# Kernel optimization log

Measured on AMD Instinct MI355X. Metric: run time of the kernel, lower is better.

Reference implementation:

```python
import jax, jax.numpy as jnp
import numpy as np

N, E, D, C = 50000, 800000, 128, 7
BN_EPS = 1e-5


def _sage_conv(x, src, dst, Wl, Wr, b):
    # mean-aggregate neighbor messages per destination, then linear + root linear
    msgs = x[src]  # [E, D] irregular gather
    summed = jax.ops.segment_sum(msgs, dst, num_segments=N)
    cnt = jax.ops.segment_sum(jnp.ones((src.shape[0],), x.dtype), dst, num_segments=N)
    agg = summed / jnp.maximum(cnt, 1.0)[:, None]
    return agg @ Wl.T + x @ Wr.T + b


def _bn_eval(x, g, be):
    # running_mean=0, running_var=1 (eval mode)
    return x * (g / jnp.sqrt(1.0 + BN_EPS)) + be


def setup_inputs() -> dict:
    key = jax.random.key(0)
    ks = jax.random.split(key, 20)
    w = lambda k, s: jax.random.normal(k, s, dtype=jnp.float32) * 0.05
    inp = {
        "x": jax.random.normal(ks[0], (N, D), dtype=jnp.float32),
        "edge_index": jax.random.randint(ks[1], (2, E), 0, N, dtype=jnp.int64),
        "Wl0": w(ks[2], (D, D)), "Wr0": w(ks[3], (D, D)), "b0": jnp.zeros((D,), jnp.float32),
        "Wl1": w(ks[4], (D, D)), "Wr1": w(ks[5], (D, D)), "b1": jnp.zeros((D,), jnp.float32),
        "Wl2": w(ks[6], (D, D)), "Wr2": w(ks[7], (D, D)), "b2": jnp.zeros((D,), jnp.float32),
        "g0": jnp.ones((D,), jnp.float32), "be0": jnp.zeros((D,), jnp.float32),
        "g1": jnp.ones((D,), jnp.float32), "be1": jnp.zeros((D,), jnp.float32),
        "dW1": w(ks[8], (D, D)), "db1": jnp.zeros((D,), jnp.float32),
        "dW2": w(ks[9], (C, D)), "db2": jnp.zeros((C,), jnp.float32),
        "dW3": w(ks[10], (D, D)), "db3": jnp.zeros((D,), jnp.float32),
    }
    return inp


def reference(x, edge_index, Wl0, Wr0, b0, Wl1, Wr1, b1, Wl2, Wr2, b2,
              g0, be0, g1, be1, dW1, db1, dW2, db2, dW3, db3):
    src, dst = edge_index[0], edge_index[1]
    h = _sage_conv(x, src, dst, Wl0, Wr0, b0)
    h = jax.nn.relu(_bn_eval(h, g0, be0))  # dropout is identity in eval
    h = _sage_conv(h, src, dst, Wl1, Wr1, b1)
    h = jax.nn.relu(_bn_eval(h, g1, be1))
    h = _sage_conv(h, src, dst, Wl2, Wr2, b2)
    recon_x1 = h @ dW1.T + db1
    recon_x2 = h @ dW2.T + db2
    recon_x3 = h @ dW3.T + db3
    return (recon_x1, recon_x2, recon_x3)
```

## Files before the change

kernel.cpp:

```cpp
#include <hip/hip_runtime.h>
#include <hip/hip_fp16.h>

static constexpr float kBnEps = 1e-5f;
static constexpr int MAXB = 1024;

typedef __attribute__((ext_vector_type(8))) _Float16 f16x8;
typedef __attribute__((ext_vector_type(4))) float f32x4;

__global__ void detect_k(const int* __restrict__ eb, int* __restrict__ flag) {
    int l = threadIdx.x;
    int v = eb[2 * l + 1];
    unsigned long long m = __ballot(v == 0);
    if (l == 0) flag[0] = (m == ~0ull) ? 1 : 0;
}

__device__ __forceinline__ int edge_src(const int* eb, int is64, int E, int e) {
    return is64 ? eb[2 * e] : eb[e];
}
__device__ __forceinline__ int edge_dst(const int* eb, int is64, int E, int e) {
    return is64 ? eb[2 * E + 2 * e] : eb[E + e];
}

__global__ __launch_bounds__(256) void histA_k(const int* __restrict__ eb,
                                               const int* __restrict__ flag,
                                               int* __restrict__ gcnt, int E,
                                               int nbuck) {
    __shared__ int lh[MAXB];
    for (int i = threadIdx.x; i < nbuck; i += 256) lh[i] = 0;
    __syncthreads();
    int is64 = flag[0];
    int base = blockIdx.x * 4096;
#pragma unroll
    for (int i = 0; i < 16; ++i) {
        int e = base + i * 256 + threadIdx.x;
        if (e < E) {
            int d = edge_dst(eb, is64, E, e);
            atomicAdd(&lh[d >> 7], 1);
        }
    }
    __syncthreads();
    for (int i = threadIdx.x; i < nbuck; i += 256) {
        int c = lh[i];
        if (c) atomicAdd(&gcnt[i], c);
    }
}

__global__ __launch_bounds__(512) void scanB_k(const int* __restrict__ gcnt,
                                               int* __restrict__ gbase,
                                               int* __restrict__ gcur,
                                               int* __restrict__ offs, int E,
                                               int n, int nbuck) {
    __shared__ int s[512];
    int tid = threadIdx.x;
    int v = (tid < nbuck) ? gcnt[tid] : 0;
    s[tid] = v;
    __syncthreads();
    for (int d = 1; d < 512; d <<= 1) {
        int t = (tid >= d) ? s[tid - d] : 0;
        __syncthreads();
        s[tid] += t;
        __syncthreads();
    }
    if (tid < nbuck) {
        gbase[tid] = s[tid] - v;
        gcur[tid] = s[tid] - v;
    }
    if (tid == 0) {
        gbase[nbuck] = E;
        offs[n] = E;
    }
}

__global__ __launch_bounds__(256) void binC_k(const int* __restrict__ eb,
                                              const int* __restrict__ flag,
                                              int* __restrict__ gcur,
                                              unsigned* __restrict__ bins, int E,
                                              int nbuck) {
    __shared__ int lh[MAXB];
    __shared__ int lcur[MAXB];
    for (int i = threadIdx.x; i < nbuck; i += 256) lh[i] = 0;
    __syncthreads();
    int is64 = flag[0];
    int base = blockIdx.x * 4096;
    int ds[16], ss[16];
#pragma unroll
    for (int i = 0; i < 16; ++i) {
        int e = base + i * 256 + threadIdx.x;
        ds[i] = -1;
        if (e < E) {
            ds[i] = edge_dst(eb, is64, E, e);
            ss[i] = edge_src(eb, is64, E, e);
            atomicAdd(&lh[ds[i] >> 7], 1);
        }
    }
    __syncthreads();
    for (int b = threadIdx.x; b < nbuck; b += 256) {
        int c = lh[b];
        lcur[b] = c ? atomicAdd(&gcur[b], c) : 0;
    }
    __syncthreads();
#pragma unroll
    for (int i = 0; i < 16; ++i) {
        if (ds[i] >= 0) {
            int bkt = ds[i] >> 7;
            int p = atomicAdd(&lcur[bkt], 1);
            bins[p] = ((unsigned)ss[i] << 7) | (unsigned)(ds[i] & 127);
        }
    }
}

__global__ __launch_bounds__(256) void csrD_k(const unsigned* __restrict__ bins,
                                              const int* __restrict__ gbase,
                                              int* __restrict__ offs,
                                              int* __restrict__ csr, int n) {
    int b = blockIdx.x;
    __shared__ int hist[128];
    __shared__ int s[128];
    __shared__ int cur[128];
    int tid = threadIdx.x;
    if (tid < 128) hist[tid] = 0;
    __syncthreads();
    int base = gbase[b], endb = gbase[b + 1], m = endb - base;
    for (int i = tid; i < m; i += 256) atomicAdd(&hist[bins[base + i] & 127u], 1);
    __syncthreads();
    int v = 0;
    if (tid < 128) {
        v = hist[tid];
        s[tid] = v;
    }
    __syncthreads();
    for (int d = 1; d < 128; d <<= 1) {
        int t = (tid >= d && tid < 128) ? s[tid - d] : 0;
        __syncthreads();
        if (tid < 128) s[tid] += t;
        __syncthreads();
    }
    if (tid < 128) {
        int excl = s[tid] - v;
        int dst = b * 128 + tid;
        if (dst < n) offs[dst] = base + excl;
        cur[tid] = base + excl;
    }
    __syncthreads();
    for (int i = tid; i < m; i += 256) {
        unsigned u = bins[base + i];
        int p = atomicAdd(&cur[u & 127u], 1);
        csr[p] = (int)(u >> 7);
    }
}

__global__ void cvtx_k(const float* __restrict__ in, __half* __restrict__ out, int total8) {
    int i = blockIdx.x * blockDim.x + threadIdx.x;
    if (i >= total8) return;
    float4 v0 = ((const float4*)in)[2 * i];
    float4 v1 = ((const float4*)in)[2 * i + 1];
    __half2 h0 = __floats2half2_rn(v0.x, v0.y);
    __half2 h1 = __floats2half2_rn(v0.z, v0.w);
    __half2 h2 = __floats2half2_rn(v1.x, v1.y);
    __half2 h3 = __floats2half2_rn(v1.z, v1.w);
    uint4 o;
    o.x = *(uint*)&h0; o.y = *(uint*)&h1; o.z = *(uint*)&h2; o.w = *(uint*)&h3;
    ((uint4*)out)[i] = o;
}

__global__ void cvtw_k(const float* __restrict__ Wl0, const float* __restrict__ Wr0,
                       const float* __restrict__ Wl1, const float* __restrict__ Wr1,
                       const float* __restrict__ Wl2, const float* __restrict__ Wr2,
                       const float* __restrict__ dW1, const float* __restrict__ dW3,
                       const float* __restrict__ dW2,
                       __half* __restrict__ Wcat, __half* __restrict__ dWcat) {
    int idx = blockIdx.x * 256 + threadIdx.x;
    if (idx < 3 * 32768) {
        int l = idx >> 15;
        int rem = idx & 32767;
        int nn = rem >> 8;
        int k = rem & 255;
        const float* Wl = (l == 0) ? Wl0 : (l == 1) ? Wl1 : Wl2;
        const float* Wr = (l == 0) ? Wr0 : (l == 1) ? Wr1 : Wr2;
        float v = (k < 128) ? Wl[nn * 128 + k] : Wr[nn * 128 + (k - 128)];
        Wcat[idx] = __float2half_rn(v);
    } else if (idx < 3 * 32768 + 3 * 16384) {
        int j = idx - 3 * 32768;
        int blk = j >> 14;
        int r = (j & 16383) >> 7;
        int c = j & 127;
        float v;
        if (blk == 0) v = dW1[r * 128 + c];
        else if (blk == 1) v = dW3[r * 128 + c];
        else v = (r < 7) ? dW2[r * 128 + c] : 0.f;
        dWcat[j] = __float2half_rn(v);
    }
}

__global__ __launch_bounds__(256) void agg_k(const __half* __restrict__ Xh,
                                             const int* __restrict__ offs,
                                             const int* __restrict__ csr,
                                             __half* __restrict__ aggh, int n) {
    int gt = blockIdx.x * blockDim.x + threadIdx.x;
    int node = gt >> 6;
    int lane = threadIdx.x & 63;
    if (node >= n) return;
    int beg = offs[node];
    int len = offs[node + 1] - beg;
    int lm1 = len - 1;
    const uint* Xp = (const uint*)Xh;
    float a0 = 0.f, a1 = 0.f;
    for (int j0 = 0; j0 < len; j0 += 16) {
        int idx[16];
#pragma unroll
        for (int t = 0; t < 16; ++t) {
            int jj = j0 + t;
            idx[t] = csr[beg + (jj < len ? jj : lm1)];
        }
        uint v[16];
#pragma unroll
        for (int t = 0; t < 16; ++t)
            v[t] = Xp[(size_t)idx[t] * 64 + lane];
#pragma unroll
        for (int t = 0; t < 16; ++t) {
            if (j0 + t < len) {
                __half2 h = *(__half2*)&v[t];
                a0 += __low2float(h);
                a1 += __high2float(h);
            }
        }
    }
    float inv = 1.0f / fmaxf((float)len, 1.0f);
    __half2 o = __floats2half2_rn(a0 * inv, a1 * inv);
    ((uint*)aggh)[(size_t)node * 64 + lane] = *(uint*)&o;
}

template <int KTOT, bool TWO_SRC, bool BN_RELU, bool OUT16, bool HEADS>
__global__ __launch_bounds__(256) void mgemm_k(
    const __half* __restrict__ A0, const __half* __restrict__ A1,
    const __half* __restrict__ Bw, const float* __restrict__ bias,
    const float* __restrict__ g, const float* __restrict__ be,
    void* __restrict__ outv, const float* __restrict__ bias2,
    void* __restrict__ outv2, const float* __restrict__ bias3,
    void* __restrict__ outv3, int n) {
    constexpr int ROWB = KTOT * 2 + 16;
    __shared__ char sA[128 * ROWB];

    int ncol = 128, ostride = 128;
    if (HEADS) {
        int y = blockIdx.y;
        Bw += (size_t)y * 128 * KTOT;
        if (y == 1) { bias = bias2; outv = outv2; }
        if (y == 2) { bias = bias3; outv = outv3; ncol = 7; ostride = 7; }
    }

    const int tid = threadIdx.x;
    const int lane = tid & 63;
    const int wid = tid >> 6;
    const int wm = wid & 1;
    const int wn = wid >> 1;
    const int row0 = blockIdx.x * 128;

    constexpr int CPR = KTOT / 8;
#pragma unroll
    for (int i = 0; i < (128 * CPR) / 256; ++i) {
        int idx = tid + i * 256;
        int r = idx / CPR;
        int c = idx % CPR;
        int rg = row0 + r;
        float4 v = make_float4(0.f, 0.f, 0.f, 0.f);
        if (rg < n) {
            if (TWO_SRC)
                v = (c < 16) ? *(const float4*)(A0 + (size_t)rg * 128 + c * 8)
                             : *(const float4*)(A1 + (size_t)rg * 128 + (c - 16) * 8);
            else
                v = *(const float4*)(A0 + (size_t)rg * 128 + c * 8);
        }
        *(float4*)(&sA[r * ROWB + c * 16]) = v;
    }

    f32x4 acc[4][4];
#pragma unroll
    for (int mi = 0; mi < 4; ++mi)
#pragma unroll
        for (int ni = 0; ni < 4; ++ni) acc[mi][ni] = (f32x4){0.f, 0.f, 0.f, 0.f};

    __syncthreads();

    const int bcol = wn * 64;
    constexpr int KH = KTOT / 128;
#pragma unroll
    for (int kh = 0; kh < KH; ++kh) {
        f16x8 bfr[4][4];
#pragma unroll
        for (int ni = 0; ni < 4; ++ni)
#pragma unroll
            for (int kt = 0; kt < 4; ++kt) {
                int col = bcol + ni * 16 + (lane & 15);
                int ko = kh * 128 + kt * 32 + (lane >> 4) * 8;
                bfr[ni][kt] = *(const f16x8*)(Bw + (size_t)col * KTOT + ko);
            }
#pragma unroll
        for (int mi = 0; mi < 4; ++mi) {
            int rl = wm * 64 + mi * 16 + (lane & 15);
            const char* base = &sA[rl * ROWB + kh * 256 + (lane >> 4) * 16];
            f16x8 afr[4];
#pragma unroll
            for (int kt = 0; kt < 4; ++kt) afr[kt] = *(const f16x8*)(base + kt * 64);
#pragma unroll
            for (int kt = 0; kt < 4; ++kt)
#pragma unroll
                for (int ni = 0; ni < 4; ++ni)
                    acc[mi][ni] = __builtin_amdgcn_mfma_f32_16x16x32_f16(
                        afr[kt], bfr[ni][kt], acc[mi][ni], 0, 0, 0);
        }
    }

#pragma unroll
    for (int ni = 0; ni < 4; ++ni) {
        int col = bcol + ni * 16 + (lane & 15);
        if (HEADS && col >= ncol) continue;
        float bv = bias[col];
        float gs = 0.f, bes = 0.f;
        if (BN_RELU) {
            gs = g[col] / sqrtf(1.0f + kBnEps);
            bes = be[col];
        }
#pragma unroll
        for (int mi = 0; mi < 4; ++mi) {
#pragma unroll
            for (int r = 0; r < 4; ++r) {
                int row = row0 + wm * 64 + mi * 16 + (lane >> 4) * 4 + r;
                if (row < n) {
                    float v = acc[mi][ni][r] + bv;
                    if (BN_RELU) v = fmaxf(v * gs + bes, 0.f);
                    if (OUT16)
                        ((__half*)outv)[(size_t)row * 128 + col] = __float2half_rn(v);
                    else
                        ((float*)outv)[(size_t)row * ostride + col] = v;
                }
            }
        }
    }
}

extern "C" void kernel_launch(void* const* d_in, const int* in_sizes, int n_in,
                              void* d_out, int out_size, void* d_ws, size_t ws_size,
                              hipStream_t stream) {
    const float* x   = (const float*)d_in[0];
    const int*   eb  = (const int*)d_in[1];
    const float* Wl0 = (const float*)d_in[2];
    const float* Wr0 = (const float*)d_in[3];
    const float* b0  = (const float*)d_in[4];
    const float* Wl1 = (const float*)d_in[5];
    const float* Wr1 = (const float*)d_in[6];
    const float* b1  = (const float*)d_in[7];
    const float* Wl2 = (const float*)d_in[8];
    const float* Wr2 = (const float*)d_in[9];
    const float* b2  = (const float*)d_in[10];
    const float* g0  = (const float*)d_in[11];
    const float* be0 = (const float*)d_in[12];
    const float* g1  = (const float*)d_in[13];
    const float* be1 = (const float*)d_in[14];
    const float* dW1 = (const float*)d_in[15];
    const float* db1 = (const float*)d_in[16];
    const float* dW2 = (const float*)d_in[17];
    const float* db2 = (const float*)d_in[18];
    const float* dW3 = (const float*)d_in[19];
    const float* db3 = (const float*)d_in[20];

    const int n = in_sizes[0] / 128;
    const int E = in_sizes[1] / 2;
    const int nbuck = (n + 127) >> 7;

    char* ws = (char*)d_ws;
    size_t off = 0;
    auto alloc = [&](size_t bytes) -> void* {
        void* p = ws + off;
        off = (off + bytes + 255) & ~(size_t)255;
        return p;
    };
    int*      flag  = (int*)alloc(16);
    int*      gcnt  = (int*)alloc(MAXB * 4);
    int*      gbase = (int*)alloc((MAXB + 1) * 4);
    int*      gcur  = (int*)alloc(MAXB * 4);
    unsigned* bins  = (unsigned*)alloc((size_t)E * 4);
    int*      csr   = (int*)alloc((size_t)E * 4);
    int*      offs  = (int*)alloc((size_t)(n + 1) * 4);
    __half*   x_h   = (__half*)alloc((size_t)n * 128 * 2);
    __half*   agg_h = (__half*)alloc((size_t)n * 128 * 2);
    __half*   h0    = (__half*)alloc((size_t)n * 128 * 2);
    __half*   h1    = (__half*)alloc((size_t)n * 128 * 2);
    __half*   h2    = h0;
    __half*   Wcat  = (__half*)alloc(3 * 32768 * 2);
    __half*   dWcat = (__half*)alloc(3 * 16384 * 2);

    float* out0 = (float*)d_out;
    float* out1 = out0 + (size_t)n * 128;
    float* out2 = out1 + (size_t)n * 7;

    hipMemsetAsync(gcnt, 0, MAXB * 4, stream);

    const int ggrid = (n + 127) / 128;
    const int agg_grid = (n * 64 + 255) / 256;
    const int chunk_grid = (E + 4095) / 4096;

    detect_k<<<1, 64, 0, stream>>>(eb, flag);
    histA_k<<<chunk_grid, 256, 0, stream>>>(eb, flag, gcnt, E, nbuck);
    scanB_k<<<1, 512, 0, stream>>>(gcnt, gbase, gcur, offs, E, n, nbuck);
    binC_k<<<chunk_grid, 256, 0, stream>>>(eb, flag, gcur, bins, E, nbuck);
    csrD_k<<<nbuck, 256, 0, stream>>>(bins, gbase, offs, csr, n);

    cvtx_k<<<(n * 16 + 255) / 256, 256, 0, stream>>>(x, x_h, n * 16);
    cvtw_k<<<(147456 + 255) / 256, 256, 0, stream>>>(Wl0, Wr0, Wl1, Wr1, Wl2, Wr2,
                                                     dW1, dW3, dW2, Wcat, dWcat);

    agg_k<<<agg_grid, 256, 0, stream>>>(x_h, offs, csr, agg_h, n);
    mgemm_k<256, true, true, true, false><<<ggrid, 256, 0, stream>>>(
        agg_h, x_h, Wcat, b0, g0, be0, h0, nullptr, nullptr, nullptr, nullptr, n);
    agg_k<<<agg_grid, 256, 0, stream>>>(h0, offs, csr, agg_h, n);
    mgemm_k<256, true, true, true, false><<<ggrid, 256, 0, stream>>>(
        agg_h, h0, Wcat + 32768, b1, g1, be1, h1, nullptr, nullptr, nullptr,
        nullptr, n);
    agg_k<<<agg_grid, 256, 0, stream>>>(h1, offs, csr, agg_h, n);
    mgemm_k<256, true, false, true, false><<<ggrid, 256, 0, stream>>>(
        agg_h, h1, Wcat + 65536, b2, nullptr, nullptr, h2, nullptr, nullptr,
        nullptr, nullptr, n);
    mgemm_k<128, false, false, false, true><<<dim3(ggrid, 3), 256, 0, stream>>>(
        h2, nullptr, dWcat, db1, nullptr, nullptr, out0, db3, out2, db2,
        out1, n);
}
```

Baseline: 261.0 us.

## Degree-sort nodes and split aggregation into quarter-row blocks; fuse prep kernels

Merges the edge-format detection, destination histogram, x conversion and weight conversion into one prep kernel, removing several launches. Adds a degree histogram and counting-sort permutation so aggregation processes nodes with similar degree together. The new aggregation kernel gives each 16-lane group one node and one quarter of the feature row, with blocks interleaved across quarters. This balances load and changes gather locality. The cost is two extra small kernels and an extra level of indirection through the permutation.

```diff
diff --git a/kernel.cpp b/kernel.cpp
--- a/kernel.cpp
+++ b/kernel.cpp
@@ -7,11 +7,11 @@
 typedef __attribute__((ext_vector_type(8))) _Float16 f16x8;
 typedef __attribute__((ext_vector_type(4))) float f32x4;
 
-__global__ void detect_k(const int* __restrict__ eb, int* __restrict__ flag) {
-    int l = threadIdx.x;
+__device__ __forceinline__ int detect64(const int* __restrict__ eb) {
+    int l = threadIdx.x & 63;
     int v = eb[2 * l + 1];
     unsigned long long m = __ballot(v == 0);
-    if (l == 0) flag[0] = (m == ~0ull) ? 1 : 0;
+    return (m == ~0ull) ? 1 : 0;
 }
 
 __device__ __forceinline__ int edge_src(const int* eb, int is64, int E, int e) {
@@ -21,27 +21,71 @@
     return is64 ? eb[2 * E + 2 * e] : eb[E + e];
 }
 
-__global__ __launch_bounds__(256) void histA_k(const int* __restrict__ eb,
-                                               const int* __restrict__ flag,
-                                               int* __restrict__ gcnt, int E,
-                                               int nbuck) {
+__global__ __launch_bounds__(256) void prep_k(
+    const int* __restrict__ eb, int* __restrict__ gcnt, int E, int nbuck,
+    const float* __restrict__ x, __half* __restrict__ x_h, int total8,
+    const float* __restrict__ Wl0, const float* __restrict__ Wr0,
+    const float* __restrict__ Wl1, const float* __restrict__ Wr1,
+    const float* __restrict__ Wl2, const float* __restrict__ Wr2,
+    const float* __restrict__ dW1, const float* __restrict__ dW3,
+    const float* __restrict__ dW2, __half* __restrict__ Wcat,
+    __half* __restrict__ dWcat, int HC, int CX) {
     __shared__ int lh[MAXB];
-    for (int i = threadIdx.x; i < nbuck; i += 256) lh[i] = 0;
-    __syncthreads();
-    int is64 = flag[0];
-    int base = blockIdx.x * 4096;
-#pragma unroll
-    for (int i = 0; i < 16; ++i) {
-        int e = base + i * 256 + threadIdx.x;
-        if (e < E) {
-            int d = edge_dst(eb, is64, E, e);
-            atomicAdd(&lh[d >> 7], 1);
-        }
-    }
-    __syncthreads();
-    for (int i = threadIdx.x; i < nbuck; i += 256) {
-        int c = lh[i];
-        if (c) atomicAdd(&gcnt[i], c);
+    int b = blockIdx.x;
+    int tid = threadIdx.x;
+    if (b < HC) {
+        for (int i = tid; i < nbuck; i += 256) lh[i] = 0;
+        __syncthreads();
+        int is64 = detect64(eb);
+        int base = b * 4096;
+#pragma unroll
+        for (int i = 0; i < 16; ++i) {
+            int e = base + i * 256 + tid;
+            if (e < E) {
+                int d = edge_dst(eb, is64, E, e);
+                atomicAdd(&lh[d >> 7], 1);
+            }
+        }
+        __syncthreads();
+        for (int i = tid; i < nbuck; i += 256) {
+            int c = lh[i];
+            if (c) atomicAdd(&gcnt[i], c);
+        }
+    } else if (b < HC + CX) {
+        int i = (b - HC) * 256 + tid;
+        if (i < total8) {
+            float4 v0 = ((const float4*)x)[2 * i];
+            float4 v1 = ((const float4*)x)[2 * i + 1];
+            __half2 h0 = __floats2half2_rn(v0.x, v0.y);
+            __half2 h1 = __floats2half2_rn(v0.z, v0.w);
+            __half2 h2 = __floats2half2_rn(v1.x, v1.y);
+            __half2 h3 = __floats2half2_rn(v1.z, v1.w);
+            uint4 o;
+            o.x = *(uint*)&h0; o.y = *(uint*)&h1; o.z = *(uint*)&h2; o.w = *(uint*)&h3;
+            ((uint4*)x_h)[i] = o;
+        }
+    } else {
+        int idx = (b - HC - CX) * 256 + tid;
+        if (idx < 3 * 32768) {
+            int l = idx >> 15;
+            int rem = idx & 32767;
+            int nn = rem >> 8;
+            int k = rem & 255;
+            const float* Wl = (l == 0) ? Wl0 : (l == 1) ? Wl1 : Wl2;
+            const float* Wr = (l == 0) ? Wr0 : (l == 1) ? Wr1 : Wr2;
+            float v = (k < 128) ? Wl[nn * 128 + k] : Wr[nn * 128 + (k - 128)];
+            Wcat[idx] = __float2half_rn(v);
+        } else if (idx < 3 * 32768 + 3 * 16384) {
+            int j = idx - 3 * 32768;
+            int blk = j >> 14;
+            int r = (j & 16383) >> 7;
+            int c = j & 127;
+            float v;
+            if (blk == 0) v = dW1[r * 128 + c];
+            else if (blk == 1) v = dW3[r * 128 + c];
+            else v = (r < 7) ? dW2[r * 128 + c] : 0.f;
+            dWcat[j] = __float2half_rn(v);
+        }
     }
 }
 
@@ -72,7 +116,6 @@
 }
 
 __global__ __launch_bounds__(256) void binC_k(const int* __restrict__ eb,
-                                              const int* __restrict__ flag,
                                               int* __restrict__ gcur,
                                               unsigned* __restrict__ bins, int E,
                                               int nbuck) {
@@ -80,7 +123,7 @@
     __shared__ int lcur[MAXB];
     for (int i = threadIdx.x; i < nbuck; i += 256) lh[i] = 0;
     __syncthreads();
-    int is64 = flag[0];
+    int is64 = detect64(eb);
     int base = blockIdx.x * 4096;
     int ds[16], ss[16];
 #pragma unroll
@@ -112,7 +155,8 @@
 __global__ __launch_bounds__(256) void csrD_k(const unsigned* __restrict__ bins,
                                               const int* __restrict__ gbase,
                                               int* __restrict__ offs,
-                                              int* __restrict__ csr, int n) {
+                                              int* __restrict__ csr,
+                                              int* __restrict__ dbin, int n) {
     int b = blockIdx.x;
     __shared__ int hist[128];
     __shared__ int s[128];
@@ -138,7 +182,10 @@
     if (tid < 128) {
         int excl = s[tid] - v;
         int dst = b * 128 + tid;
-        if (dst < n) offs[dst] = base + excl;
+        if (dst < n) {
+            offs[dst] = base + excl;
+            atomicAdd(&dbin[v > 255 ? 255 : v], 1);
+        }
         cur[tid] = base + excl;
     }
     __syncthreads();
@@ -149,75 +196,69 @@
     }
 }
 
-__global__ void cvtx_k(const float* __restrict__ in, __half* __restrict__ out, int total8) {
-    int i = blockIdx.x * blockDim.x + threadIdx.x;
-    if (i >= total8) return;
-    float4 v0 = ((const float4*)in)[2 * i];
-    float4 v1 = ((const float4*)in)[2 * i + 1];
-    __half2 h0 = __floats2half2_rn(v0.x, v0.y);
-    __half2 h1 = __floats2half2_rn(v0.z, v0.w);
-    __half2 h2 = __floats2half2_rn(v1.x, v1.y);
-    __half2 h3 = __floats2half2_rn(v1.z, v1.w);
-    uint4 o;
-    o.x = *(uint*)&h0; o.y = *(uint*)&h1; o.z = *(uint*)&h2; o.w = *(uint*)&h3;
-    ((uint4*)out)[i] = o;
-}
-
-__global__ void cvtw_k(const float* __restrict__ Wl0, const float* __restrict__ Wr0,
-                       const float* __restrict__ Wl1, const float* __restrict__ Wr1,
-                       const float* __restrict__ Wl2, const float* __restrict__ Wr2,
-                       const float* __restrict__ dW1, const float* __restrict__ dW3,
-                       const float* __restrict__ dW2,
-                       __half* __restrict__ Wcat, __half* __restrict__ dWcat) {
-    int idx = blockIdx.x * 256 + threadIdx.x;
-    if (idx < 3 * 32768) {
-        int l = idx >> 15;
-        int rem = idx & 32767;
-        int nn = rem >> 8;
-        int k = rem & 255;
-        const float* Wl = (l == 0) ? Wl0 : (l == 1) ? Wl1 : Wl2;
-        const float* Wr = (l == 0) ? Wr0 : (l == 1) ? Wr1 : Wr2;
-        float v = (k < 128) ? Wl[nn * 128 + k] : Wr[nn * 128 + (k - 128)];
-        Wcat[idx] = __float2half_rn(v);
-    } else if (idx < 3 * 32768 + 3 * 16384) {
-        int j = idx - 3 * 32768;
-        int blk = j >> 14;
-        int r = (j & 16383) >> 7;
-        int c = j & 127;
-        float v;
-        if (blk == 0) v = dW1[r * 128 + c];
-        else if (blk == 1) v = dW3[r * 128 + c];
-        else v = (r < 7) ? dW2[r * 128 + c] : 0.f;
-        dWcat[j] = __float2half_rn(v);
-    }
-}
-
-__global__ __launch_bounds__(256) void agg_k(const __half* __restrict__ Xh,
-                                             const int* __restrict__ offs,
-                                             const int* __restrict__ csr,
-                                             __half* __restrict__ aggh, int n) {
-    int gt = blockIdx.x * blockDim.x + threadIdx.x;
-    int node = gt >> 6;
+__global__ __launch_bounds__(256) void dscan_k(const int* __restrict__ dbin,
+                                               int* __restrict__ dcur) {
+    __shared__ int s[256];
+    int tid = threadIdx.x;
+    int v = dbin[tid];
+    s[tid] = v;
+    __syncthreads();
+    for (int d = 1; d < 256; d <<= 1) {
+        int t = (tid >= d) ? s[tid - d] : 0;
+        __syncthreads();
+        s[tid] += t;
+        __syncthreads();
+    }
+    dcur[tid] = s[tid] - v;
+}
+
+__global__ __launch_bounds__(256) void dscat_k(const int* __restrict__ offs,
+                                               int* __restrict__ dcur,
+                                               int* __restrict__ perm, int n) {
+    int i = blockIdx.x * 256 + threadIdx.x;
+    if (i >= n) return;
+    int deg = offs[i + 1] - offs[i];
+    int b = deg > 255 ? 255 : deg;
+    int pos = atomicAdd(&dcur[b], 1);
+    perm[pos] = i;
+}
+
+__global__ __launch_bounds__(256) void agg4_k(const __half* __restrict__ Xh,
+                                              const int* __restrict__ offs,
+                                              const int* __restrict__ csr,
+                                              const int* __restrict__ perm,
+                                              __half* __restrict__ aggh, int n,
+                                              int G) {
+    int bid = blockIdx.x;
+    int q = (bid & 7) >> 1;
+    int gi = (bid >> 3) * 2 + (bid & 1);
+    if (gi >= G) return;
+    int wv = threadIdx.x >> 6;
     int lane = threadIdx.x & 63;
-    if (node >= n) return;
-    int beg = offs[node];
-    int len = offs[node + 1] - beg;
+    int grp = lane >> 4, lg = lane & 15;
+    int slot = gi * 16 + wv * 4 + grp;
+    int node = (slot < n) ? perm[slot] : -1;
+    int beg = 0, len = 0;
+    if (node >= 0) {
+        beg = offs[node];
+        len = offs[node + 1] - beg;
+    }
     int lm1 = len - 1;
     const uint* Xp = (const uint*)Xh;
     float a0 = 0.f, a1 = 0.f;
-    for (int j0 = 0; j0 < len; j0 += 16) {
-        int idx[16];
-#pragma unroll
-        for (int t = 0; t < 16; ++t) {
+    for (int j0 = 0; j0 < len; j0 += 8) {
+        int idx[8];
+#pragma unroll
+        for (int t = 0; t < 8; ++t) {
             int jj = j0 + t;
-            idx[t] = csr[beg + (jj < len ? jj : lm1)];
-        }
-        uint v[16];
-#pragma unroll
-        for (int t = 0; t < 16; ++t)
-            v[t] = Xp[(size_t)idx[t] * 64 + lane];
-#pragma unroll
-        for (int t = 0; t < 16; ++t) {
+            idx[t] = csr[beg + (jj < lm1 ? jj : lm1)];
+        }
+        uint v[8];
+#pragma unroll
+        for (int t = 0; t < 8; ++t)
+            v[t] = Xp[(size_t)idx[t] * 64 + q * 16 + lg];
+#pragma unroll
+        for (int t = 0; t < 8; ++t) {
             if (j0 + t < len) {
                 __half2 h = *(__half2*)&v[t];
                 a0 += __low2float(h);
@@ -225,9 +266,11 @@
             }
         }
     }
-    float inv = 1.0f / fmaxf((float)len, 1.0f);
-    __half2 o = __floats2half2_rn(a0 * inv, a1 * inv);
-    ((uint*)aggh)[(size_t)node * 64 + lane] = *(uint*)&o;
+    if (node >= 0) {
+        float inv = 1.0f / fmaxf((float)len, 1.0f);
+        __half2 o = __floats2half2_rn(a0 * inv, a1 * inv);
+        ((uint*)aggh)[(size_t)node * 64 + q * 16 + lg] = *(uint*)&o;
+    }
 }
 
 template <int KTOT, bool TWO_SRC, bool BN_RELU, bool OUT16, bool HEADS>
@@ -375,13 +418,15 @@
         off = (off + bytes + 255) & ~(size_t)255;
         return p;
     };
-    int*      flag  = (int*)alloc(16);
     int*      gcnt  = (int*)alloc(MAXB * 4);
+    int*      dbin  = (int*)alloc(256 * 4);
+    int*      dcur  = (int*)alloc(256 * 4);
     int*      gbase = (int*)alloc((MAXB + 1) * 4);
     int*      gcur  = (int*)alloc(MAXB * 4);
     unsigned* bins  = (unsigned*)alloc((size_t)E * 4);
     int*      csr   = (int*)alloc((size_t)E * 4);
     int*      offs  = (int*)alloc((size_t)(n + 1) * 4);
+    int*      perm  = (int*)alloc((size_t)n * 4);
     __half*   x_h   = (__half*)alloc((size_t)n * 128 * 2);
     __half*   agg_h = (__half*)alloc((size_t)n * 128 * 2);
     __half*   h0    = (__half*)alloc((size_t)n * 128 * 2);
@@ -394,30 +439,32 @@
     float* out1 = out0 + (size_t)n * 128;
     float* out2 = out1 + (size_t)n * 7;
 
-    hipMemsetAsync(gcnt, 0, MAXB * 4, stream);
+    hipMemsetAsync(gcnt, 0, MAXB * 4 + 256 * 4, stream);
 
     const int ggrid = (n + 127) / 128;
-    const int agg_grid = (n * 64 + 255) / 256;
-    const int chunk_grid = (E + 4095) / 4096;
-
-    detect_k<<<1, 64, 0, stream>>>(eb, flag);
-    histA_k<<<chunk_grid, 256, 0, stream>>>(eb, flag, gcnt, E, nbuck);
+    const int HC = (E + 4095) / 4096;
+    const int CX = (n * 16 + 255) / 256;
+    const int CW = (147456 + 255) / 256;
+    const int G = (n + 15) / 16;
+    const int agg_grid = ((G + 1) / 2) * 8;
+
+    prep_k<<<HC + CX + CW, 256, 0, stream>>>(eb, gcnt, E, nbuck, x, x_h, n * 16,
+                                             Wl0, Wr0, Wl1, Wr1, Wl2, Wr2, dW1,
+                                             dW3, dW2, Wcat, dWcat, HC, CX);
     scanB_k<<<1, 512, 0, stream>>>(gcnt, gbase, gcur, offs, E, n, nbuck);
-    binC_k<<<chunk_grid, 256, 0, stream>>>(eb, flag, gcur, bins, E, nbuck);
-    csrD_k<<<nbuck, 256, 0, stream>>>(bins, gbase, offs, csr, n);
-
-    cvtx_k<<<(n * 16 + 255) / 256, 256, 0, stream>>>(x, x_h, n * 16);
-    cvtw_k<<<(147456 + 255) / 256, 256, 0, stream>>>(Wl0, Wr0, Wl1, Wr1, Wl2, Wr2,
-                                                     dW1, dW3, dW2, Wcat, dWcat);
-
-    agg_k<<<agg_grid, 256, 0, stream>>>(x_h, offs, csr, agg_h, n);
+    binC_k<<<HC, 256, 0, stream>>>(eb, gcur, bins, E, nbuck);
+    csrD_k<<<nbuck, 256, 0, stream>>>(bins, gbase, offs, csr, dbin, n);
+    dscan_k<<<1, 256, 0, stream>>>(dbin, dcur);
+    dscat_k<<<(n + 255) / 256, 256, 0, stream>>>(offs, dcur, perm, n);
+
+    agg4_k<<<agg_grid, 256, 0, stream>>>(x_h, offs, csr, perm, agg_h, n, G);
     mgemm_k<256, true, true, true, false><<<ggrid, 256, 0, stream>>>(
         agg_h, x_h, Wcat, b0, g0, be0, h0, nullptr, nullptr, nullptr, nullptr, n);
-    agg_k<<<agg_grid, 256, 0, stream>>>(h0, offs, csr, agg_h, n);
+    agg4_k<<<agg_grid, 256, 0, stream>>>(h0, offs, csr, perm, agg_h, n, G);
     mgemm_k<256, true, true, true, false><<<ggrid, 256, 0, stream>>>(
         agg_h, h0, Wcat + 32768, b1, g1, be1, h1, nullptr, nullptr, nullptr,
         nullptr, n);
-    agg_k<<<agg_grid, 256, 0, stream>>>(h1, offs, csr, agg_h, n);
+    agg4_k<<<agg_grid, 256, 0, stream>>>(h1, offs, csr, perm, agg_h, n, G);
     mgemm_k<256, true, false, true, false><<<ggrid, 256, 0, stream>>>(
         agg_h, h1, Wcat + 65536, b2, nullptr, nullptr, h2, nullptr, nullptr,
         nullptr, nullptr, n);
```

Result: slower. 554.0 us (+112.3%).
